# Kernel optimization log

Hardware: AMD Instinct MI355X
Metric: run time of the kernel (lower is better)

The kernel has to match this reference:

```python
import math
import jax, jax.numpy as jnp
import numpy as np
from jax import lax

B = 8
IN_CH = 512
OUT_CH = 256
K = 3
LATENT = 512
BLUR = [1, 3, 3, 1]
FACTOR = 2
H = W = 64
# p = len(blur) - factor - (K-1) = 0 -> pad = ((p+1)//2 + factor - 1, p//2 + 1) = (1, 1)
PAD0, PAD1 = 1, 1


def _make_blur_kernel():
    k = jnp.array(BLUR, jnp.float32)
    k = k[None, :] * k[:, None]          # separable -> 2D
    k = k / jnp.sum(k)
    return k * (FACTOR ** 2)             # make_kernel(blur, factor) scales by factor^2


def setup_inputs() -> dict:
    key = jax.random.key(0)
    k1, k2, k3, k4 = jax.random.split(key, 4)
    inputs = {
        "input": jax.random.normal(k1, (B, IN_CH, H, W), jnp.float32),
        "w": jax.random.normal(k2, (B, LATENT), jnp.float32),
        # learned params
        "affine_weight": jax.random.normal(k3, (IN_CH, LATENT), jnp.float32),
        "affine_bias": jnp.ones((IN_CH,), jnp.float32),  # bias_init=1
        "conv_weight": jax.random.normal(k4, (1, OUT_CH, IN_CH, K, K), jnp.float32),
    }
    return inputs


def reference(input, w, affine_weight, affine_bias, conv_weight):
    batch = input.shape[0]
    # EqualLinear: scale = 1/sqrt(latent_dim), lr_mul=1
    style = w @ (affine_weight * (1.0 / math.sqrt(LATENT))).T + affine_bias  # (B, IN_CH)
    # modulate
    scale = 1.0 / math.sqrt(IN_CH * K * K)
    weight = (scale * conv_weight) * style[:, None, :, None, None]          # (B, OUT, IN, K, K)
    # demodulate over (in, kh, kw)
    demod = lax.rsqrt(jnp.sum(weight * weight, axis=(2, 3, 4)) + 1e-8)      # (B, OUT)
    weight = weight * demod[:, :, None, None, None]
    # grouped conv_transpose2d (groups=batch, stride=2, pad=0) == per-sample
    # conv with lhs_dilation=2, spatial padding K-1, kernel spatially flipped.
    kflip = jnp.flip(weight, (-2, -1))                                      # (B, OUT, IN, K, K) OIHW

    def ct(x, kern):  # x: (IN, H, W), kern: (OUT, IN, K, K)
        return lax.conv_general_dilated(
            x[None], kern, window_strides=(1, 1),
            padding=[(K - 1, K - 1), (K - 1, K - 1)],
            lhs_dilation=(2, 2),
            dimension_numbers=("NCHW", "OIHW", "NCHW"))[0]

    out = jax.vmap(ct)(input, kflip)                                        # (B, OUT, 2H-2+K, 2W-2+K)
    # upfirdn2d with up=down=1: pad then depthwise correlate with flipped FIR kernel
    blur = jnp.flip(_make_blur_kernel())                                    # (4, 4)
    out = jnp.pad(out, ((0, 0), (0, 0), (PAD0, PAD1), (PAD0, PAD1)))
    dw = jnp.tile(blur[None, None], (OUT_CH, 1, 1, 1))                      # (OUT, 1, 4, 4)
    out = lax.conv_general_dilated(
        out, dw, window_strides=(1, 1), padding="VALID",
        feature_group_count=OUT_CH,
        dimension_numbers=("NCHW", "OIHW", "NCHW"))
    return out  # (B, OUT, 2H, 2W)
```

## Files before the change

kernel.cpp:

```cpp
#include <hip/hip_runtime.h>
#include <hip/hip_bf16.h>
#include <math.h>

#define NB 8
#define INCH 512
#define OUTCH 256
#define SP 4096
#define LAT 512
#define NTAP 9
#define MDIM (NTAP*OUTCH)

#define INV_SQRT_LAT 0.044194173824159216f
#define WSCALE 0.014731391274719738f

typedef __bf16 bf16x8 __attribute__((ext_vector_type(8)));
typedef float  f32x4  __attribute__((ext_vector_type(4)));

__device__ __forceinline__ unsigned short f2bf(float f) {
  unsigned u = __float_as_uint(f);
  u += 0x7fffu + ((u >> 16) & 1u);
  return (unsigned short)(u >> 16);
}
__device__ __forceinline__ float bf2f(unsigned short v) {
  return __uint_as_float((unsigned)v << 16);
}

__global__ void prep_k(const float* __restrict__ w, const float* __restrict__ aff,
                       const float* __restrict__ bias, float* __restrict__ style,
                       const float* __restrict__ cw, float* __restrict__ S,
                       unsigned short* __restrict__ w9) {
  if (blockIdx.x < 16) {
    int gid = blockIdx.x * 256 + threadIdx.x;
    int b = gid >> 9, i = gid & 511;
    const float4* wv = (const float4*)(w + (size_t)b * LAT);
    const float4* av = (const float4*)(aff + (size_t)i * LAT);
    float s = 0.f;
#pragma unroll 4
    for (int l = 0; l < LAT / 4; ++l) {
      float4 a = av[l], ww = wv[l];
      s += a.x * ww.x + a.y * ww.y + a.z * ww.z + a.w * ww.w;
    }
    style[gid] = s * INV_SQRT_LAT + bias[i];
  } else {
    int gid = (blockIdx.x - 16) * 256 + threadIdx.x;
    int o = gid >> 9, i = gid & 511;
    const float* p = cw + (size_t)gid * 9;
    float ss = 0.f, v[9];
#pragma unroll
    for (int t = 0; t < 9; ++t) { v[t] = p[t]; ss += v[t] * v[t]; }
    S[gid] = ss * (WSCALE * WSCALE);
#pragma unroll
    for (int t = 0; t < 9; ++t)
      w9[((size_t)(t * OUTCH + o)) * INCH + i] = f2bf(v[t] * WSCALE);
  }
}

__global__ void demod_k(const float* __restrict__ style, const float* __restrict__ S,
                        float* __restrict__ dmod) {
  int gid = blockIdx.x * 256 + threadIdx.x;
  int b = gid >> 8, o = gid & 255;
  const float4* sv = (const float4*)(style + (size_t)b * INCH);
  const float4* Sv = (const float4*)(S + (size_t)o * INCH);
  float acc = 0.f;
#pragma unroll 4
  for (int l = 0; l < INCH / 4; ++l) {
    float4 st = sv[l], s2 = Sv[l];
    acc += st.x * st.x * s2.x + st.y * st.y * s2.y + st.z * st.z * s2.z + st.w * st.w * s2.w;
  }
  dmod[gid] = 1.0f / sqrtf(acc + 1e-8f);
}

__global__ void modx_k(const float* __restrict__ x, const float* __restrict__ style,
                       unsigned short* __restrict__ xmt) {
  __shared__ float tile[32][33];
  int b = blockIdx.z;
  int s0 = blockIdx.x * 32;
  int i0 = blockIdx.y * 32;
  int c = threadIdx.x & 31, r = threadIdx.x >> 5;
#pragma unroll
  for (int p = 0; p < 4; ++p) {
    int ii = r + p * 8;
    tile[ii][c] = x[((size_t)(b * INCH + i0 + ii)) * SP + s0 + c] * style[b * INCH + i0 + ii];
  }
  __syncthreads();
#pragma unroll
  for (int p = 0; p < 4; ++p) {
    int ss = r + p * 8;
    xmt[((size_t)(b * SP + s0 + ss)) * INCH + i0 + c] = f2bf(tile[c][ss]);
  }
}

__global__ __launch_bounds__(512, 2)
void gemm_k(const unsigned short* __restrict__ A,
            const unsigned short* __restrict__ Bm,
            unsigned short* __restrict__ C) {
  __shared__ __align__(16) unsigned short lds[65536];
  Bm += (size_t)blockIdx.z * SP * INCH;
  C  += (size_t)blockIdx.z * MDIM * SP;
  const int tid  = threadIdx.x;
  const int lane = tid & 63;
  const int wid  = tid >> 6;
  const int wr   = wid >> 2;
  const int wc   = wid & 3;
  const int m0 = blockIdx.y * 256;
  const int n0 = blockIdx.x * 256;
  const int r16  = lane & 15;
  const int quad = lane >> 4;
  const int xorv = r16 & 7;
  const int ch0 = ((0 + quad) ^ xorv) * 8;
  const int ch1 = ((4 + quad) ^ xorv) * 8;
  const int aBase = (wr * 128 + r16) * 64;
  const int bBase = (wc * 64 + r16) * 64;

  const int srow = tid >> 3;
  const int sgch = ((tid & 7) ^ (srow & 7)) * 8;
  const int swb  = wid * 512;

  f32x4 acc[8][4];
#pragma unroll
  for (int i = 0; i < 8; ++i)
#pragma unroll
    for (int j = 0; j < 4; ++j) acc[i][j] = (f32x4){0.f, 0.f, 0.f, 0.f};

#define STAGE_TILE(T) do {                                                          \
    const int _buf = (T) & 1;                                                       \
    const int _k0  = (T) * 64;                                                      \
    unsigned short* _la = &lds[_buf * 16384 + swb];                                 \
    unsigned short* _lb = &lds[32768 + _buf * 16384 + swb];                         \
    const unsigned short* _ga = A  + (size_t)(m0 + srow) * INCH + _k0 + sgch;       \
    const unsigned short* _gb = Bm + (size_t)(n0 + srow) * INCH + _k0 + sgch;       \
    _Pragma("unroll")                                                               \
    for (int _it = 0; _it < 4; ++_it) {                                             \
      __builtin_amdgcn_global_load_lds(                                             \
          (const __attribute__((address_space(1))) void*)(_ga + (size_t)_it * 64 * INCH), \
          (__attribute__((address_space(3))) void*)(_la + _it * 4096), 16, 0, 0);   \
      __builtin_amdgcn_global_load_lds(                                             \
          (const __attribute__((address_space(1))) void*)(_gb + (size_t)_it * 64 * INCH), \
          (__attribute__((address_space(3))) void*)(_lb + _it * 4096), 16, 0, 0);   \
    }                                                                               \
  } while (0)

#define READ_A(MH) do {                                                             \
    _Pragma("unroll")                                                               \
    for (int _i = 0; _i < 4; ++_i) {                                                \
      const int _rb = aBase + ((MH) * 64 + _i * 16) * 64;                           \
      af[0][_i] = *(const bf16x8*)&As_[_rb + ch0];                                  \
      af[1][_i] = *(const bf16x8*)&As_[_rb + ch1];                                  \
    }                                                                               \
  } while (0)

#define READ_B(NH) do {                                                             \
    _Pragma("unroll")                                                               \
    for (int _j = 0; _j < 2; ++_j) {                                                \
      const int _rb = bBase + ((NH) * 32 + _j * 16) * 64;                           \
      bfr[0][_j] = *(const bf16x8*)&Bs_[_rb + ch0];                                 \
      bfr[1][_j] = *(const bf16x8*)&Bs_[_rb + ch1];                                 \
    }                                                                               \
  } while (0)

#define MFMA_Q(MH, NH) do {                                                         \
    __builtin_amdgcn_s_setprio(1);                                                  \
    _Pragma("unroll")                                                               \
    for (int _kk = 0; _kk < 2; ++_kk)                                               \
    _Pragma("unroll")                                                               \
    for (int _i = 0; _i < 4; ++_i)                                                  \
    _Pragma("unroll")                                                               \
    for (int _j = 0; _j < 2; ++_j)                                                  \
      acc[(MH)*4+_i][(NH)*2+_j] = __builtin_amdgcn_mfma_f32_16x16x32_bf16(          \
          af[_kk][_i], bfr[_kk][_j], acc[(MH)*4+_i][(NH)*2+_j], 0, 0, 0);           \
    __builtin_amdgcn_s_setprio(0);                                                  \
  } while (0)

  STAGE_TILE(0);
  STAGE_TILE(1);
  asm volatile("s_waitcnt vmcnt(8)" ::: "memory");
  __builtin_amdgcn_sched_barrier(0);
  __builtin_amdgcn_s_barrier();

  for (int t = 0; t < 8; ++t) {
    const unsigned short* As_ = &lds[(t & 1) * 16384];
    const unsigned short* Bs_ = &lds[32768 + (t & 1) * 16384];
    bf16x8 af[2][4], bfr[2][2];
    if (t >= 1 && t <= 6) STAGE_TILE(t + 1);
    READ_A(0); READ_B(0);
    __builtin_amdgcn_s_barrier();
    MFMA_Q(0, 0);
    __builtin_amdgcn_s_barrier();
    READ_B(1);
    __builtin_amdgcn_s_barrier();
    MFMA_Q(0, 1);
    __builtin_amdgcn_s_barrier();
    READ_A(1);
    __builtin_amdgcn_s_barrier();
    MFMA_Q(1, 1);
    __builtin_amdgcn_s_barrier();
    READ_B(0);
    __builtin_amdgcn_s_barrier();
    MFMA_Q(1, 0);
    if (t < 7) {
      asm volatile("s_waitcnt vmcnt(0)" ::: "memory");
      __builtin_amdgcn_sched_barrier(0);
    }
    __builtin_amdgcn_s_barrier();
  }
#undef STAGE_TILE
#undef READ_A
#undef READ_B
#undef MFMA_Q

#pragma unroll
  for (int i = 0; i < 8; ++i)
#pragma unroll
    for (int j = 0; j < 4; ++j)
#pragma unroll
      for (int r = 0; r < 4; ++r) {
        int row = wr * 128 + i * 16 + quad * 4 + r;
        int col = wc * 64 + j * 16 + r16;
        int pc  = (col >> 3) ^ (row & 31);
        lds[row * 256 + pc * 8 + (col & 7)] = f2bf(acc[i][j][r]);
      }
  __syncthreads();
#pragma unroll
  for (int rr = 0; rr < 16; ++rr) {
    int row = rr * 16 + (tid >> 5);
    int c   = tid & 31;
    int pc  = c ^ (row & 31);
    uint4 v = *(const uint4*)&lds[row * 256 + pc * 8];
    *(uint4*)&C[(size_t)(m0 + row) * SP + n0 + c * 8] = v;
  }
}

#define STRIP 8
#define TLSTR 70
#define TLROWS 10
__global__ __launch_bounds__(256)
void combine_k(const unsigned short* __restrict__ T, const float* __restrict__ dm,
               float* __restrict__ out) {
  __shared__ __align__(16) unsigned short TlB[9 * TLROWS * TLSTR + 4];
  __shared__ __align__(16) float V[3 * TLROWS * 128];
  T   += (size_t)blockIdx.z * MDIM * SP;
  dm  += (size_t)blockIdx.z * OUTCH;
  out += (size_t)blockIdx.z * OUTCH * 128 * 128;
  const int o  = blockIdx.y;
  const int Y0 = blockIdx.x * STRIP;
  const int tid = threadIdx.x;

  {
    uint4* tz = (uint4*)TlB;
#pragma unroll
    for (int idx = tid; idx < 788; idx += 256) tz[idx] = (uint4){0u, 0u, 0u, 0u};
  }
  __syncthreads();

  for (int idx = tid; idx < 1440; idx += 256) {
    int tap = idx / 160;
    int rem = idx - tap * 160;
    int ry  = rem >> 4;
    int c16 = rem & 15;
    int Yg = Y0 - 1 + ry;
    if ((unsigned)Yg < 64u) {
      ushort4 v4 = *(const ushort4*)(T + (size_t)(tap * OUTCH + o) * SP + Yg * 64 + c16 * 4);
      unsigned short* dst = &TlB[(tap * TLROWS + ry) * TLSTR + 4 + c16 * 4];
      *(ushort2*)(dst)     = make_ushort2(v4.x, v4.y);
      *(ushort2*)(dst + 2) = make_ushort2(v4.z, v4.w);
    }
  }
  __syncthreads();

  {
    const int r  = tid >> 3;
    const int xc = tid & 7;
    if (r < 30) {
      const int c  = r / 10;
      const int yr = r - c * 10;
      const int X0 = xc * 8;
      float td[3][12];
#pragma unroll
      for (int d = 0; d < 3; ++d) {
        const unsigned short* src = &TlB[((c * 3 + d) * TLROWS + yr) * TLSTR + 2 + X0];
#pragma unroll
        for (int k = 0; k < 6; ++k) {
          ushort2 u2 = *(const ushort2*)(src + 2 * k);
          td[d][2 * k]     = bf2f(u2.x);
          td[d][2 * k + 1] = bf2f(u2.y);
        }
      }
      float vout[16];
#pragma unroll
      for (int Xl = 0; Xl < 8; ++Xl) {
        float a0 = td[0][Xl + 1], a1 = td[0][Xl + 2], a2 = td[0][Xl + 3];
        float b0 = td[1][Xl + 1], b1 = td[1][Xl + 2], b2 = td[1][Xl + 3];
        float c0 = td[2][Xl + 1], c1 = td[2][Xl + 2], c2 = td[2][Xl + 3];
        vout[2 * Xl]     = b0 + 3.f * c0 + 3.f * a1 + 3.f * b1 + c1 + a2;
        vout[2 * Xl + 1] = c0 + a1 + 3.f * b1 + 3.f * c1 + 3.f * a2 + b2;
      }
      float* vr = &V[(c * TLROWS + yr) * 128];
#pragma unroll
      for (int j = 0; j < 4; ++j) {
        int l = 4 * xc + j;
        int p = (l & ~3) | ((l & 3) ^ ((l >> 3) & 3));
        *(f32x4*)(vr + p * 4) = (f32x4){vout[4 * j], vout[4 * j + 1], vout[4 * j + 2], vout[4 * j + 3]};
      }
    }
  }
  __syncthreads();

  {
    const int y  = tid >> 4;
    const int py = y & 1;
    const int Yl = y >> 1;
    const float dmv = dm[o] * (1.0f / 16.0f);
    float* orow = out + ((size_t)o * 128 + (Y0 * 2 + y)) * 128;
#pragma unroll
    for (int xg = 0; xg < 2; ++xg) {
      int l = (tid & 15) + 16 * xg;
      int p = (l & ~3) | ((l & 3) ^ ((l >> 3) & 3));
      int off = p * 4;
      f32x4 v00 = *(const f32x4*)&V[((0 * TLROWS) + Yl + 0) * 128 + off];
      f32x4 v01 = *(const f32x4*)&V[((0 * TLROWS) + Yl + 1) * 128 + off];
      f32x4 v02 = *(const f32x4*)&V[((0 * TLROWS) + Yl + 2) * 128 + off];
      f32x4 v10 = *(const f32x4*)&V[((1 * TLROWS) + Yl + 0) * 128 + off];
      f32x4 v11 = *(const f32x4*)&V[((1 * TLROWS) + Yl + 1) * 128 + off];
      f32x4 v12 = *(const f32x4*)&V[((1 * TLROWS) + Yl + 2) * 128 + off];
      f32x4 v20 = *(const f32x4*)&V[((2 * TLROWS) + Yl + 0) * 128 + off];
      f32x4 v21 = *(const f32x4*)&V[((2 * TLROWS) + Yl + 1) * 128 + off];
      f32x4 v22 = *(const f32x4*)&V[((2 * TLROWS) + Yl + 2) * 128 + off];
      f32x4 r;
      if (py == 0)
        r = v10 + 3.f * v20 + 3.f * v01 + 3.f * v11 + v21 + v02;
      else
        r = v20 + v01 + 3.f * v11 + 3.f * v21 + 3.f * v02 + v12;
      r *= dmv;
      *(f32x4*)(orow + l * 4) = r;
    }
  }
}

extern "C" void kernel_launch(void* const* d_in, const int* in_sizes, int n_in,
                              void* d_out, int out_size, void* d_ws, size_t ws_size,
                              hipStream_t stream) {
  const float* x    = (const float*)d_in[0];
  const float* w    = (const float*)d_in[1];
  const float* aff  = (const float*)d_in[2];
  const float* bias = (const float*)d_in[3];
  const float* cw   = (const float*)d_in[4];
  float* out = (float*)d_out;
  char* ws = (char*)d_ws;
  float* style        = (float*)(ws);
  float* S            = (float*)(ws + 16384);
  float* dmod         = (float*)(ws + 540672);
  unsigned short* w9  = (unsigned short*)(ws + 548864);
  unsigned short* xmt = (unsigned short*)(ws + 2908160);
  unsigned short* T   = (unsigned short*)(ws + 36462592);

  hipLaunchKernelGGL(prep_k, dim3(528), dim3(256), 0, stream, w, aff, bias, style, cw, S, w9);
  hipLaunchKernelGGL(demod_k, dim3(8), dim3(256), 0, stream, style, S, dmod);
  hipLaunchKernelGGL(modx_k, dim3(128, 16, 8), dim3(256), 0, stream, x, style, xmt);
  hipLaunchKernelGGL(gemm_k, dim3(16, 9, NB), dim3(512), 0, stream, w9, xmt, T);
  hipLaunchKernelGGL(combine_k, dim3(64 / STRIP, 256, NB), dim3(256), 0, stream, T, dmod, out);
}
```

Measured before the change: 403.1 us.

## Switch GEMM mainloop to 4-stage K=32 pipeline with split A/B staging

The bf16 GEMM mainloop moves from a double-buffered K=64 tile to a four-buffer ring of K=32 tiles, prefetched three steps ahead, with A and B loads issued in separate phases of each iteration. The LDS swizzle is redone for 32-element rows, and the four MFMA quadrants with their barriers are reduced to two phases per step. The goal is deeper prefetch and fewer barriers per MFMA so global-load latency is hidden better. In exchange there are twice as many loop iterations with less MFMA work each, and more vmcnt bookkeeping that must stay correct.

```diff
diff --git a/kernel.cpp b/kernel.cpp
--- a/kernel.cpp
+++ b/kernel.cpp
@@ -106,15 +106,10 @@
   const int n0 = blockIdx.x * 256;
   const int r16  = lane & 15;
   const int quad = lane >> 4;
-  const int xorv = r16 & 7;
-  const int ch0 = ((0 + quad) ^ xorv) * 8;
-  const int ch1 = ((4 + quad) ^ xorv) * 8;
-  const int aBase = (wr * 128 + r16) * 64;
-  const int bBase = (wc * 64 + r16) * 64;
-
-  const int srow = tid >> 3;
-  const int sgch = ((tid & 7) ^ (srow & 7)) * 8;
+
+  const int srow = tid >> 2;
   const int swb  = wid * 512;
+  const int sgch = ((tid & 3) ^ ((srow >> 2) & 3)) * 8;
 
   f32x4 acc[8][4];
 #pragma unroll
@@ -122,91 +117,93 @@
 #pragma unroll
     for (int j = 0; j < 4; ++j) acc[i][j] = (f32x4){0.f, 0.f, 0.f, 0.f};
 
-#define STAGE_TILE(T) do {                                                          \
-    const int _buf = (T) & 1;                                                       \
-    const int _k0  = (T) * 64;                                                      \
-    unsigned short* _la = &lds[_buf * 16384 + swb];                                 \
-    unsigned short* _lb = &lds[32768 + _buf * 16384 + swb];                         \
-    const unsigned short* _ga = A  + (size_t)(m0 + srow) * INCH + _k0 + sgch;       \
-    const unsigned short* _gb = Bm + (size_t)(n0 + srow) * INCH + _k0 + sgch;       \
-    _Pragma("unroll")                                                               \
-    for (int _it = 0; _it < 4; ++_it) {                                             \
-      __builtin_amdgcn_global_load_lds(                                             \
-          (const __attribute__((address_space(1))) void*)(_ga + (size_t)_it * 64 * INCH), \
-          (__attribute__((address_space(3))) void*)(_la + _it * 4096), 16, 0, 0);   \
-      __builtin_amdgcn_global_load_lds(                                             \
-          (const __attribute__((address_space(1))) void*)(_gb + (size_t)_it * 64 * INCH), \
-          (__attribute__((address_space(3))) void*)(_lb + _it * 4096), 16, 0, 0);   \
-    }                                                                               \
-  } while (0)
-
-#define READ_A(MH) do {                                                             \
+#define STAGE_A(T) do {                                                             \
+    unsigned short* _la = &lds[((T) & 3) * 8192 + swb];                             \
+    const unsigned short* _ga = A + (size_t)(m0 + srow) * INCH + (T) * 32 + sgch;   \
+    __builtin_amdgcn_global_load_lds(                                               \
+        (const __attribute__((address_space(1))) void*)_ga,                         \
+        (__attribute__((address_space(3))) void*)_la, 16, 0, 0);                    \
+    __builtin_amdgcn_global_load_lds(                                               \
+        (const __attribute__((address_space(1))) void*)(_ga + (size_t)128 * INCH),  \
+        (__attribute__((address_space(3))) void*)(_la + 4096), 16, 0, 0);           \
+  } while (0)
+
+#define STAGE_B(T) do {                                                             \
+    unsigned short* _lb = &lds[32768 + ((T) & 3) * 8192 + swb];                     \
+    const unsigned short* _gb = Bm + (size_t)(n0 + srow) * INCH + (T) * 32 + sgch;  \
+    __builtin_amdgcn_global_load_lds(                                               \
+        (const __attribute__((address_space(1))) void*)_gb,                         \
+        (__attribute__((address_space(3))) void*)_lb, 16, 0, 0);                    \
+    __builtin_amdgcn_global_load_lds(                                               \
+        (const __attribute__((address_space(1))) void*)(_gb + (size_t)128 * INCH),  \
+        (__attribute__((address_space(3))) void*)(_lb + 4096), 16, 0, 0);           \
+  } while (0)
+
+#define READ_A(PH) do {                                                             \
     _Pragma("unroll")                                                               \
     for (int _i = 0; _i < 4; ++_i) {                                                \
-      const int _rb = aBase + ((MH) * 64 + _i * 16) * 64;                           \
-      af[0][_i] = *(const bf16x8*)&As_[_rb + ch0];                                  \
-      af[1][_i] = *(const bf16x8*)&As_[_rb + ch1];                                  \
+      const int _ra = wr * 128 + ((PH) * 4 + _i) * 16 + r16;                        \
+      af[_i] = *(const bf16x8*)&As_[_ra * 32 + ((quad ^ ((_ra >> 2) & 3)) * 8)];    \
     }                                                                               \
   } while (0)
 
-#define READ_B(NH) do {                                                             \
+#define READ_B() do {                                                               \
     _Pragma("unroll")                                                               \
-    for (int _j = 0; _j < 2; ++_j) {                                                \
-      const int _rb = bBase + ((NH) * 32 + _j * 16) * 64;                           \
-      bfr[0][_j] = *(const bf16x8*)&Bs_[_rb + ch0];                                 \
-      bfr[1][_j] = *(const bf16x8*)&Bs_[_rb + ch1];                                 \
+    for (int _j = 0; _j < 4; ++_j) {                                                \
+      const int _rb = wc * 64 + _j * 16 + r16;                                      \
+      bfv[_j] = *(const bf16x8*)&Bs_[_rb * 32 + ((quad ^ ((_rb >> 2) & 3)) * 8)];   \
     }                                                                               \
   } while (0)
 
-#define MFMA_Q(MH, NH) do {                                                         \
+#define MFMA_PH(PH) do {                                                            \
     __builtin_amdgcn_s_setprio(1);                                                  \
-    _Pragma("unroll")                                                               \
-    for (int _kk = 0; _kk < 2; ++_kk)                                               \
     _Pragma("unroll")                                                               \
     for (int _i = 0; _i < 4; ++_i)                                                  \
     _Pragma("unroll")                                                               \
-    for (int _j = 0; _j < 2; ++_j)                                                  \
-      acc[(MH)*4+_i][(NH)*2+_j] = __builtin_amdgcn_mfma_f32_16x16x32_bf16(          \
-          af[_kk][_i], bfr[_kk][_j], acc[(MH)*4+_i][(NH)*2+_j], 0, 0, 0);           \
+    for (int _j = 0; _j < 4; ++_j)                                                  \
+      acc[(PH) * 4 + _i][_j] = __builtin_amdgcn_mfma_f32_16x16x32_bf16(             \
+          af[_i], bfv[_j], acc[(PH) * 4 + _i][_j], 0, 0, 0);                        \
     __builtin_amdgcn_s_setprio(0);                                                  \
   } while (0)
 
-  STAGE_TILE(0);
-  STAGE_TILE(1);
+  STAGE_A(0); STAGE_B(0);
+  STAGE_A(1); STAGE_B(1);
+  STAGE_A(2); STAGE_B(2);
   asm volatile("s_waitcnt vmcnt(8)" ::: "memory");
   __builtin_amdgcn_sched_barrier(0);
   __builtin_amdgcn_s_barrier();
 
-  for (int t = 0; t < 8; ++t) {
-    const unsigned short* As_ = &lds[(t & 1) * 16384];
-    const unsigned short* Bs_ = &lds[32768 + (t & 1) * 16384];
-    bf16x8 af[2][4], bfr[2][2];
-    if (t >= 1 && t <= 6) STAGE_TILE(t + 1);
-    READ_A(0); READ_B(0);
+  for (int t = 0; t < 16; ++t) {
+    const unsigned short* As_ = &lds[(t & 3) * 8192];
+    const unsigned short* Bs_ = &lds[32768 + (t & 3) * 8192];
+    bf16x8 af[4], bfv[4];
+    if (t + 3 < 16) STAGE_A(t + 3);
+    READ_A(0);
+    READ_B();
     __builtin_amdgcn_s_barrier();
-    MFMA_Q(0, 0);
+    MFMA_PH(0);
     __builtin_amdgcn_s_barrier();
-    READ_B(1);
-    __builtin_amdgcn_s_barrier();
-    MFMA_Q(0, 1);
-    __builtin_amdgcn_s_barrier();
+    if (t + 3 < 16) STAGE_B(t + 3);
     READ_A(1);
     __builtin_amdgcn_s_barrier();
-    MFMA_Q(1, 1);
-    __builtin_amdgcn_s_barrier();
-    READ_B(0);
-    __builtin_amdgcn_s_barrier();
-    MFMA_Q(1, 0);
-    if (t < 7) {
+    MFMA_PH(1);
+    if (t < 13) {
+      asm volatile("s_waitcnt vmcnt(8)" ::: "memory");
+      __builtin_amdgcn_sched_barrier(0);
+    } else if (t == 13) {
+      asm volatile("s_waitcnt vmcnt(4)" ::: "memory");
+      __builtin_amdgcn_sched_barrier(0);
+    } else if (t == 14) {
       asm volatile("s_waitcnt vmcnt(0)" ::: "memory");
       __builtin_amdgcn_sched_barrier(0);
     }
     __builtin_amdgcn_s_barrier();
   }
-#undef STAGE_TILE
+#undef STAGE_A
+#undef STAGE_B
 #undef READ_A
 #undef READ_B
-#undef MFMA_Q
+#undef MFMA_PH
 
 #pragma unroll
   for (int i = 0; i < 8; ++i)
```

Result: slower. 412.7 us (+2.4%).

## Shrink GEMM N-tile to 128 and use triple-buffered staggered LDS prefetch

Applied to the files above, without the earlier changes.

The GEMM block tile goes from 256x256 to 256x128, with 8 waves arranged 4x2 each computing 64x64, which halves the accumulator registers and doubles the grid. The LDS pipeline changes from double to triple buffering, prefetching two k-tiles ahead. The global-to-LDS loads are spread across the four MFMA phases so memory traffic overlaps compute more evenly. Operand reuse per block drops and A tiles are reloaded twice as often, in exchange for better occupancy and a smoother pipeline.

```diff
diff --git a/kernel.cpp b/kernel.cpp
--- a/kernel.cpp
+++ b/kernel.cpp
@@ -94,67 +94,62 @@
 void gemm_k(const unsigned short* __restrict__ A,
             const unsigned short* __restrict__ Bm,
             unsigned short* __restrict__ C) {
-  __shared__ __align__(16) unsigned short lds[65536];
+  __shared__ __align__(16) unsigned short lds[73728];
   Bm += (size_t)blockIdx.z * SP * INCH;
   C  += (size_t)blockIdx.z * MDIM * SP;
   const int tid  = threadIdx.x;
   const int lane = tid & 63;
   const int wid  = tid >> 6;
-  const int wr   = wid >> 2;
-  const int wc   = wid & 3;
+  const int wm   = (wid >> 1) * 64;
+  const int wn   = (wid & 1) * 64;
   const int m0 = blockIdx.y * 256;
-  const int n0 = blockIdx.x * 256;
+  const int n0 = blockIdx.x * 128;
   const int r16  = lane & 15;
   const int quad = lane >> 4;
-  const int xorv = r16 & 7;
-  const int ch0 = ((0 + quad) ^ xorv) * 8;
-  const int ch1 = ((4 + quad) ^ xorv) * 8;
-  const int aBase = (wr * 128 + r16) * 64;
-  const int bBase = (wc * 64 + r16) * 64;
 
   const int srow = tid >> 3;
   const int sgch = ((tid & 7) ^ (srow & 7)) * 8;
   const int swb  = wid * 512;
 
-  f32x4 acc[8][4];
-#pragma unroll
-  for (int i = 0; i < 8; ++i)
+  f32x4 acc[4][4];
+#pragma unroll
+  for (int i = 0; i < 4; ++i)
 #pragma unroll
     for (int j = 0; j < 4; ++j) acc[i][j] = (f32x4){0.f, 0.f, 0.f, 0.f};
 
-#define STAGE_TILE(T) do {                                                          \
-    const int _buf = (T) & 1;                                                       \
-    const int _k0  = (T) * 64;                                                      \
-    unsigned short* _la = &lds[_buf * 16384 + swb];                                 \
-    unsigned short* _lb = &lds[32768 + _buf * 16384 + swb];                         \
-    const unsigned short* _ga = A  + (size_t)(m0 + srow) * INCH + _k0 + sgch;       \
-    const unsigned short* _gb = Bm + (size_t)(n0 + srow) * INCH + _k0 + sgch;       \
-    _Pragma("unroll")                                                               \
-    for (int _it = 0; _it < 4; ++_it) {                                             \
+#define STAGE_A2(T, IT0) do {                                                       \
+    unsigned short* _la = &lds[(((T) % 3) * 16384) + swb];                          \
+    const unsigned short* _ga = A + (size_t)(m0 + srow) * INCH + (T) * 64 + sgch;   \
+    _Pragma("unroll")                                                               \
+    for (int _it = (IT0); _it < (IT0) + 2; ++_it)                                   \
       __builtin_amdgcn_global_load_lds(                                             \
           (const __attribute__((address_space(1))) void*)(_ga + (size_t)_it * 64 * INCH), \
           (__attribute__((address_space(3))) void*)(_la + _it * 4096), 16, 0, 0);   \
-      __builtin_amdgcn_global_load_lds(                                             \
-          (const __attribute__((address_space(1))) void*)(_gb + (size_t)_it * 64 * INCH), \
-          (__attribute__((address_space(3))) void*)(_lb + _it * 4096), 16, 0, 0);   \
+  } while (0)
+
+#define STAGE_B1(T, IT) do {                                                        \
+    unsigned short* _lb = &lds[49152 + (((T) % 3) * 8192) + swb];                   \
+    const unsigned short* _gb = Bm + (size_t)(n0 + (IT) * 64 + srow) * INCH + (T) * 64 + sgch; \
+    __builtin_amdgcn_global_load_lds(                                               \
+        (const __attribute__((address_space(1))) void*)_gb,                         \
+        (__attribute__((address_space(3))) void*)(_lb + (IT) * 4096), 16, 0, 0);    \
+  } while (0)
+
+#define READ_A(MH) do {                                                             \
+    _Pragma("unroll")                                                               \
+    for (int _i = 0; _i < 2; ++_i) {                                                \
+      const int _ra = wm + ((MH) * 2 + _i) * 16 + r16;                              \
+      af[0][_i] = *(const bf16x8*)&As_[_ra * 64 + (((0 + quad) ^ (_ra & 7)) * 8)];  \
+      af[1][_i] = *(const bf16x8*)&As_[_ra * 64 + (((4 + quad) ^ (_ra & 7)) * 8)];  \
     }                                                                               \
   } while (0)
 
-#define READ_A(MH) do {                                                             \
-    _Pragma("unroll")                                                               \
-    for (int _i = 0; _i < 4; ++_i) {                                                \
-      const int _rb = aBase + ((MH) * 64 + _i * 16) * 64;                           \
-      af[0][_i] = *(const bf16x8*)&As_[_rb + ch0];                                  \
-      af[1][_i] = *(const bf16x8*)&As_[_rb + ch1];                                  \
-    }                                                                               \
-  } while (0)
-
 #define READ_B(NH) do {                                                             \
     _Pragma("unroll")                                                               \
     for (int _j = 0; _j < 2; ++_j) {                                                \
-      const int _rb = bBase + ((NH) * 32 + _j * 16) * 64;                           \
-      bfr[0][_j] = *(const bf16x8*)&Bs_[_rb + ch0];                                 \
-      bfr[1][_j] = *(const bf16x8*)&Bs_[_rb + ch1];                                 \
+      const int _rb = wn + ((NH) * 2 + _j) * 16 + r16;                              \
+      bfv[0][_j] = *(const bf16x8*)&Bs_[_rb * 64 + (((0 + quad) ^ (_rb & 7)) * 8)]; \
+      bfv[1][_j] = *(const bf16x8*)&Bs_[_rb * 64 + (((4 + quad) ^ (_rb & 7)) * 8)]; \
     }                                                                               \
   } while (0)
 
@@ -163,69 +158,77 @@
     _Pragma("unroll")                                                               \
     for (int _kk = 0; _kk < 2; ++_kk)                                               \
     _Pragma("unroll")                                                               \
-    for (int _i = 0; _i < 4; ++_i)                                                  \
+    for (int _i = 0; _i < 2; ++_i)                                                  \
     _Pragma("unroll")                                                               \
     for (int _j = 0; _j < 2; ++_j)                                                  \
-      acc[(MH)*4+_i][(NH)*2+_j] = __builtin_amdgcn_mfma_f32_16x16x32_bf16(          \
-          af[_kk][_i], bfr[_kk][_j], acc[(MH)*4+_i][(NH)*2+_j], 0, 0, 0);           \
+      acc[(MH)*2+_i][(NH)*2+_j] = __builtin_amdgcn_mfma_f32_16x16x32_bf16(          \
+          af[_kk][_i], bfv[_kk][_j], acc[(MH)*2+_i][(NH)*2+_j], 0, 0, 0);           \
     __builtin_amdgcn_s_setprio(0);                                                  \
   } while (0)
 
-  STAGE_TILE(0);
-  STAGE_TILE(1);
-  asm volatile("s_waitcnt vmcnt(8)" ::: "memory");
+  STAGE_A2(0, 0); STAGE_A2(0, 2); STAGE_B1(0, 0); STAGE_B1(0, 1);
+  STAGE_A2(1, 0); STAGE_A2(1, 2); STAGE_B1(1, 0); STAGE_B1(1, 1);
+  asm volatile("s_waitcnt vmcnt(6)" ::: "memory");
   __builtin_amdgcn_sched_barrier(0);
   __builtin_amdgcn_s_barrier();
 
   for (int t = 0; t < 8; ++t) {
-    const unsigned short* As_ = &lds[(t & 1) * 16384];
-    const unsigned short* Bs_ = &lds[32768 + (t & 1) * 16384];
-    bf16x8 af[2][4], bfr[2][2];
-    if (t >= 1 && t <= 6) STAGE_TILE(t + 1);
+    const unsigned short* As_ = &lds[(t % 3) * 16384];
+    const unsigned short* Bs_ = &lds[49152 + (t % 3) * 8192];
+    const bool st = (t < 6);
+    bf16x8 af[2][2], bfv[2][2];
+    if (st) STAGE_A2(t + 2, 0);
     READ_A(0); READ_B(0);
     __builtin_amdgcn_s_barrier();
     MFMA_Q(0, 0);
     __builtin_amdgcn_s_barrier();
+    if (st) STAGE_A2(t + 2, 2);
     READ_B(1);
     __builtin_amdgcn_s_barrier();
     MFMA_Q(0, 1);
     __builtin_amdgcn_s_barrier();
+    if (st) STAGE_B1(t + 2, 0);
     READ_A(1);
     __builtin_amdgcn_s_barrier();
     MFMA_Q(1, 1);
     __builtin_amdgcn_s_barrier();
+    if (st) STAGE_B1(t + 2, 1);
     READ_B(0);
     __builtin_amdgcn_s_barrier();
     MFMA_Q(1, 0);
-    if (t < 7) {
+    if (t < 6) {
+      asm volatile("s_waitcnt vmcnt(6)" ::: "memory");
+      __builtin_amdgcn_sched_barrier(0);
+    } else if (t == 6) {
       asm volatile("s_waitcnt vmcnt(0)" ::: "memory");
       __builtin_amdgcn_sched_barrier(0);
     }
     __builtin_amdgcn_s_barrier();
   }
-#undef STAGE_TILE
+#undef STAGE_A2
+#undef STAGE_B1
 #undef READ_A
 #undef READ_B
 #undef MFMA_Q
 
 #pragma unroll
-  for (int i = 0; i < 8; ++i)
+  for (int i = 0; i < 4; ++i)
 #pragma unroll
     for (int j = 0; j < 4; ++j)
 #pragma unroll
       for (int r = 0; r < 4; ++r) {
-        int row = wr * 128 + i * 16 + quad * 4 + r;
-        int col = wc * 64 + j * 16 + r16;
-        int pc  = (col >> 3) ^ (row & 31);
-        lds[row * 256 + pc * 8 + (col & 7)] = f2bf(acc[i][j][r]);
+        int row = wm + i * 16 + quad * 4 + r;
+        int col = wn + j * 16 + r16;
+        int pc  = (col >> 3) ^ (row & 15);
+        lds[row * 128 + pc * 8 + (col & 7)] = f2bf(acc[i][j][r]);
       }
   __syncthreads();
 #pragma unroll
-  for (int rr = 0; rr < 16; ++rr) {
-    int row = rr * 16 + (tid >> 5);
-    int c   = tid & 31;
-    int pc  = c ^ (row & 31);
-    uint4 v = *(const uint4*)&lds[row * 256 + pc * 8];
+  for (int rr = 0; rr < 8; ++rr) {
+    int row = rr * 32 + (tid >> 4);
+    int c   = tid & 15;
+    int pc  = c ^ (row & 15);
+    uint4 v = *(const uint4*)&lds[row * 128 + pc * 8];
     *(uint4*)&C[(size_t)(m0 + row) * SP + n0 + c * 8] = v;
   }
 }
@@ -356,6 +359,6 @@
   hipLaunchKernelGGL(prep_k, dim3(528), dim3(256), 0, stream, w, aff, bias, style, cw, S, w9);
   hipLaunchKernelGGL(demod_k, dim3(8), dim3(256), 0, stream, style, S, dmod);
   hipLaunchKernelGGL(modx_k, dim3(128, 16, 8), dim3(256), 0, stream, x, style, xmt);
-  hipLaunchKernelGGL(gemm_k, dim3(16, 9, NB), dim3(512), 0, stream, w9, xmt, T);
+  hipLaunchKernelGGL(gemm_k, dim3(32, 9, NB), dim3(512), 0, stream, w9, xmt, T);
   hipLaunchKernelGGL(combine_k, dim3(64 / STRIP, 256, NB), dim3(256), 0, stream, T, dmod, out);
 }
```

Result: no change. 396.4 us (-1.7%).
